# Performance work log

Hardware: AMD Instinct MI355X
Metric: run time of the kernel (lower is better)

## Reference

```python
import jax, jax.numpy as jnp
import numpy as np

D_MODEL = 512
NUM_HEADS = 8
D_K = D_MODEL // NUM_HEADS  # 64, also d_v
SEQ_LEN = 4096


def setup_inputs() -> dict:
    key = jax.random.key(0)
    k1, k2, k3, k4, k5 = jax.random.split(key, 5)
    scale = jnp.float32(1.0 / np.sqrt(D_MODEL))  # keep exp(scores) finite
    return {
        "embeded_seq": jax.random.normal(k1, (SEQ_LEN, D_MODEL), jnp.float32),
        "q_proj": jax.random.normal(k2, (NUM_HEADS, D_MODEL, D_K), jnp.float32) * scale,
        "k_proj": jax.random.normal(k3, (NUM_HEADS, D_MODEL, D_K), jnp.float32) * scale,
        "v_proj": jax.random.normal(k4, (NUM_HEADS, D_MODEL, D_K), jnp.float32) * scale,
        "out_proj": jax.random.normal(k5, (NUM_HEADS * D_K, D_MODEL), jnp.float32) * scale,
    }


def reference(embeded_seq, q_proj, k_proj, v_proj, out_proj):
    # Per-head linear projections: (S, D) x (H, D, d_k) -> (H, S, d_k)
    qs = jnp.einsum("sd,hdk->hsk", embeded_seq, q_proj)
    ks = jnp.einsum("sd,hdk->hsk", embeded_seq, k_proj)
    vs = jnp.einsum("sd,hdv->hsv", embeded_seq, v_proj)

    # Scores: (H, S, S), scaled by sqrt(d_k)
    scores = jnp.einsum("hsk,htk->hst", qs, ks) / jnp.float32(np.sqrt(D_K))

    # Faithful to the original: torch.sum(e_powered) is a GLOBAL scalar sum
    # over all heads and positions (a buggy "softmax"), not a row softmax.
    e = jnp.exp(scores)
    softmaxed = e / jnp.sum(e)

    # Attention output per head: (H, S, d_v)
    head_attns = jnp.einsum("hst,htv->hsv", softmaxed, vs)

    # Concat heads along feature dim -> (S, H*d_v), then output projection
    concat = jnp.transpose(head_attns, (1, 0, 2)).reshape(SEQ_LEN, NUM_HEADS * D_K)
    return concat @ out_proj
```

## Files before the change

### kernel.cpp

```cpp
#include <hip/hip_runtime.h>
#include <stdint.h>

#define S_LEN 4096
#define DMODEL 512
#define NHEAD 8
#define DK 64
#define SPLIT 4
#define TBLK 64
#define NT ((S_LEN / SPLIT) / TBLK)

#if __has_builtin(__builtin_amdgcn_exp2f)
#define EXPFN(x) __builtin_amdgcn_exp2f(x)
#define QSCALE 0.18033688011112042f
#else
#define EXPFN(x) __expf(x)
#define QSCALE 0.125f
#endif

typedef __attribute__((ext_vector_type(8))) short short8;
typedef __attribute__((ext_vector_type(4))) float f32x4;
typedef __attribute__((ext_vector_type(16))) float f32x16;
typedef __attribute__((ext_vector_type(4))) unsigned int uint4v;

__device__ __forceinline__ unsigned short f2bf(float f) {
    unsigned int u = __float_as_uint(f);
    u = (u + 0x7fffu + ((u >> 16) & 1u)) >> 16;
    return (unsigned short)u;
}

__device__ __forceinline__ void gload16(const unsigned short* g, unsigned short* l) {
    __builtin_amdgcn_global_load_lds(
        (const __attribute__((address_space(1))) unsigned int*)g,
        (__attribute__((address_space(3))) unsigned int*)l, 16, 0, 0);
}

__global__ __launch_bounds__(256) void prep_kernel(
    const float* __restrict__ emb,
    const float* __restrict__ wq, const float* __restrict__ wk, const float* __restrict__ wv,
    const float* __restrict__ wo,
    unsigned short* __restrict__ embB,
    unsigned short* __restrict__ oq, unsigned short* __restrict__ ok,
    unsigned short* __restrict__ ov, unsigned short* __restrict__ woT,
    float* __restrict__ Z) {
    __shared__ float tile[64][65];
    const int blk = blockIdx.x, tid = threadIdx.x;
    if (blk < 2048) {
        int i = blk * 256 + tid;
        if (i == 0) *Z = 0.0f;
        float4 v = reinterpret_cast<const float4*>(emb)[i];
        ushort4 o;
        o.x = f2bf(v.x); o.y = f2bf(v.y); o.z = f2bf(v.z); o.w = f2bf(v.w);
        reinterpret_cast<ushort4*>(embB)[i] = o;
        return;
    }
    const int tr = tid >> 4, tc4 = (tid & 15) * 4;
    if (blk < 2240) {
        int idx = blk - 2048;
        int xx = idx & 7, yy = idx >> 3;
        int p = yy >> 3, h = yy & 7;
        const float* in = ((p == 0) ? wq : (p == 1) ? wk : wv) + (size_t)h * DMODEL * DK;
        unsigned short* out = ((p == 0) ? oq : (p == 1) ? ok : ov) + (size_t)h * DK * DMODEL;
        int r0 = xx * 64;
#pragma unroll
        for (int rr = 0; rr < 4; ++rr) {
            float4 v = *reinterpret_cast<const float4*>(in + (size_t)(r0 + tr + rr * 16) * DK + tc4);
            tile[tr + rr * 16][tc4 + 0] = v.x;
            tile[tr + rr * 16][tc4 + 1] = v.y;
            tile[tr + rr * 16][tc4 + 2] = v.z;
            tile[tr + rr * 16][tc4 + 3] = v.w;
        }
        __syncthreads();
#pragma unroll
        for (int rr = 0; rr < 4; ++rr) {
            const int c = tr + rr * 16;
            ushort4 o;
            o.x = f2bf(tile[tc4 + 0][c]);
            o.y = f2bf(tile[tc4 + 1][c]);
            o.z = f2bf(tile[tc4 + 2][c]);
            o.w = f2bf(tile[tc4 + 3][c]);
            *reinterpret_cast<ushort4*>(out + (size_t)c * DMODEL + r0 + tc4) = o;
        }
        return;
    }
    {
        int idx = blk - 2240;
        int c0 = (idx & 7) * 64, r0 = (idx >> 3) * 64;
#pragma unroll
        for (int rr = 0; rr < 4; ++rr) {
            float4 v = *reinterpret_cast<const float4*>(wo + (size_t)(r0 + tr + rr * 16) * DMODEL + c0 + tc4);
            tile[tr + rr * 16][tc4 + 0] = v.x;
            tile[tr + rr * 16][tc4 + 1] = v.y;
            tile[tr + rr * 16][tc4 + 2] = v.z;
            tile[tr + rr * 16][tc4 + 3] = v.w;
        }
        __syncthreads();
#pragma unroll
        for (int rr = 0; rr < 4; ++rr) {
            const int c = tr + rr * 16;
            ushort4 o;
            o.x = f2bf(tile[tc4 + 0][c]);
            o.y = f2bf(tile[tc4 + 1][c]);
            o.z = f2bf(tile[tc4 + 2][c]);
            o.w = f2bf(tile[tc4 + 3][c]);
            *reinterpret_cast<ushort4*>(woT + (size_t)(c0 + c) * DMODEL + r0 + tc4) = o;
        }
    }
}

__global__ __launch_bounds__(256, 2) void proj_tiled_kernel(
    const unsigned short* __restrict__ A,
    const unsigned short* __restrict__ BTall,
    unsigned short* __restrict__ Qo,
    unsigned short* __restrict__ Ko,
    unsigned short* __restrict__ Vo) {
    __shared__ unsigned short lds[32768];
    const int tid = threadIdx.x;
    const int w = tid >> 6, l = tid & 63;
    const int l15 = l & 15, lg = l >> 4;
    const int wr = w >> 1, wc = w & 1;
    const int m0 = blockIdx.x * 128, n0 = blockIdx.y * 128;
    const int srow = l >> 3;
    const int schk = ((l & 7) ^ srow) << 3;
    f32x4 acc[4][4] = {};
    {
        unsigned short* ab = &lds[0];
        unsigned short* bb = &lds[8192];
#pragma unroll
        for (int g = 0; g < 4; ++g) {
            gload16(A + (size_t)(m0 + w * 32 + g * 8 + srow) * DMODEL + schk,
                    ab + (w * 32 + g * 8) * 64);
            gload16(BTall + (size_t)(n0 + w * 32 + g * 8 + srow) * DMODEL + schk,
                    bb + (w * 32 + g * 8) * 64);
        }
    }
    __syncthreads();
    for (int kt = 0; kt < 8; ++kt) {
        const int b = (kt & 1) * 16384;
        if (kt + 1 < 8) {
            const int nb = ((kt + 1) & 1) * 16384;
            const int k0 = (kt + 1) * 64;
            unsigned short* ab = &lds[nb];
            unsigned short* bb = &lds[nb + 8192];
#pragma unroll
            for (int g = 0; g < 4; ++g) {
                gload16(A + (size_t)(m0 + w * 32 + g * 8 + srow) * DMODEL + k0 + schk,
                        ab + (w * 32 + g * 8) * 64);
                gload16(BTall + (size_t)(n0 + w * 32 + g * 8 + srow) * DMODEL + k0 + schk,
                        bb + (w * 32 + g * 8) * 64);
            }
        }
#pragma unroll
        for (int kk = 0; kk < 2; ++kk) {
            short8 am[4], bn[4];
#pragma unroll
            for (int mi = 0; mi < 4; ++mi) {
                const int row = wr * 64 + mi * 16 + l15;
                am[mi] = *reinterpret_cast<const short8*>(
                    &lds[b + row * 64 + ((kk * 32 + lg * 8) ^ ((row & 7) << 3))]);
            }
#pragma unroll
            for (int ni = 0; ni < 4; ++ni) {
                const int row = wc * 64 + ni * 16 + l15;
                bn[ni] = *reinterpret_cast<const short8*>(
                    &lds[b + 8192 + row * 64 + ((kk * 32 + lg * 8) ^ ((row & 7) << 3))]);
            }
#pragma unroll
            for (int mi = 0; mi < 4; ++mi)
#pragma unroll
                for (int ni = 0; ni < 4; ++ni)
                    acc[mi][ni] = __builtin_amdgcn_mfma_f32_16x16x32_bf16(am[mi], bn[ni], acc[mi][ni], 0, 0, 0);
        }
        __syncthreads();
    }
#pragma unroll
    for (int ni = 0; ni < 4; ++ni) {
        const int n = n0 + wc * 64 + ni * 16;
        const int p = n >> 9, h = (n >> 6) & 7, vb = n & 63;
        unsigned short* dst = ((p == 0) ? Qo : (p == 1) ? Ko : Vo) + (size_t)h * S_LEN * DK;
        const float sc = (p == 0) ? QSCALE : 1.0f;
#pragma unroll
        for (int mi = 0; mi < 4; ++mi) {
            const int s = m0 + wr * 64 + mi * 16 + lg * 4;
#pragma unroll
            for (int r = 0; r < 4; ++r)
                dst[(size_t)(s + r) * DK + vb + l15] = f2bf(acc[mi][ni][r] * sc);
        }
    }
}

__global__ __launch_bounds__(256) void vt_kernel(const unsigned short* __restrict__ Vb,
                                                 unsigned short* __restrict__ VT) {
    __shared__ unsigned short tile[4096];
    int h = blockIdx.y, t0 = blockIdx.x * 64;
    const unsigned short* Vh = Vb + h * (S_LEN * DK);
    unsigned short* VTh = VT + h * (DK * S_LEN);
    int c8 = (threadIdx.x & 7) * 8, rw = threadIdx.x >> 3;
#pragma unroll
    for (int rr = 0; rr < 2; ++rr) {
        int t = rw + rr * 32;
        short8 v = *reinterpret_cast<const short8*>(Vh + (t0 + t) * DK + c8);
        *reinterpret_cast<short8*>(&tile[t * 64 + (c8 ^ ((t & 7) << 3))]) = v;
    }
    __syncthreads();
    const int g16 = c8 & ~15;
    const int h4 = (c8 & 8) ? 4 : 0;
#pragma unroll
    for (int rr = 0; rr < 2; ++rr) {
        int v = rw + rr * 32;
        short8 s;
#pragma unroll
        for (int i = 0; i < 8; ++i) {
            int t = g16 + h4 + ((i < 4) ? i : (i + 4));
            s[i] = (short)tile[t * 64 + (v ^ ((t & 7) << 3))];
        }
        *reinterpret_cast<short8*>(VTh + v * S_LEN + t0 + c8) = s;
    }
}

__device__ __forceinline__ void make_pfrag(const f32x16& s, short8 pf[2],
                                           float& z0, float& z1) {
    float p[16];
#pragma unroll
    for (int r = 0; r < 16; ++r) p[r] = EXPFN(s[r]);
#pragma unroll
    for (int r = 0; r < 16; r += 2) { z0 += p[r]; z1 += p[r + 1]; }
    unsigned int c[8];
#pragma unroll
    for (int j = 0; j < 8; ++j)
        asm("v_cvt_pk_bf16_f32 %0, %1, %2" : "=v"(c[j]) : "v"(p[2 * j]), "v"(p[2 * j + 1]));
    uint4v wa = {c[0], c[1], c[2], c[3]};
    uint4v wb = {c[4], c[5], c[6], c[7]};
    pf[0] = __builtin_bit_cast(short8, wa);
    pf[1] = __builtin_bit_cast(short8, wb);
}

__global__ __launch_bounds__(256, 2) void attn_kernel(
    const unsigned short* __restrict__ Qg,
    const unsigned short* __restrict__ Kg,
    const unsigned short* __restrict__ VTg,
    unsigned short* __restrict__ Opart,
    float* __restrict__ Z) {
    __shared__ unsigned short lds[16384];
    const int tid = threadIdx.x;
    const int w = tid >> 6, l = tid & 63;
    const int l31 = l & 31, lh = l >> 5;
    const int vx = l31 & 7;
    const int qb = blockIdx.x, h = blockIdx.y, sp = blockIdx.z;
    const unsigned short* Qh = Qg + h * (S_LEN * DK);
    const unsigned short* Kh = Kg + h * (S_LEN * DK);
    const unsigned short* VTh = VTg + h * (DK * S_LEN);
    const int t_base = sp * (S_LEN / SPLIT);
    const int q0 = qb * 256 + w * 64;

    short8 bq[2][4];
#pragma unroll
    for (int qc = 0; qc < 2; ++qc)
#pragma unroll
        for (int ks = 0; ks < 4; ++ks)
            bq[qc][ks] = *reinterpret_cast<const short8*>(
                Qh + (q0 + qc * 32 + l31) * DK + ks * 16 + lh * 8);

    f32x16 oacc[2][2] = {};
    float z0 = 0.0f, z1 = 0.0f;

    const int srow = l >> 3;
    const int scol = ((l & 7) ^ srow) << 3;
    const unsigned short* gk = Kh + (size_t)(t_base + w * 16 + srow) * DK + scol;
    const unsigned short* gv0 = VTh + (size_t)(w * 16 + srow) * S_LEN + t_base + scol;
    const unsigned short* gv1 = gv0 + 8 * S_LEN;

    {
        unsigned short* kb = &lds[w * 1024];
        gload16(gk, kb);
        gload16(gk + 512, kb + 512);
        unsigned short* vb = &lds[4096 + w * 1024];
        gload16(gv0, vb);
        gload16(gv1, vb + 512);
        gk += 64 * DK; gv0 += 64; gv1 += 64;
    }
    __syncthreads();

    for (int it = 0; it < NT; ++it) {
        const int b = (it & 1) * 8192;
        if (it + 1 < NT) {
            const int nb = ((it + 1) & 1) * 8192;
            unsigned short* kb = &lds[nb + w * 1024];
            gload16(gk, kb);
            gload16(gk + 512, kb + 512);
            unsigned short* vb = &lds[nb + 4096 + w * 1024];
            gload16(gv0, vb);
            gload16(gv1, vb + 512);
            gk += 64 * DK; gv0 += 64; gv1 += 64;
        }
#pragma unroll
        for (int tc = 0; tc < 2; ++tc) {
            f32x16 s0 = {}, s1 = {};
            const int tA = tc * 32 + l31;
            __builtin_amdgcn_s_setprio(1);
#pragma unroll
            for (int ks = 0; ks < 4; ++ks) {
                short8 ka = *reinterpret_cast<const short8*>(
                    &lds[b + tA * 64 + ((ks * 16 + lh * 8) ^ ((tA & 7) << 3))]);
                s0 = __builtin_amdgcn_mfma_f32_32x32x16_bf16(ka, bq[0][ks], s0, 0, 0, 0);
                s1 = __builtin_amdgcn_mfma_f32_32x32x16_bf16(ka, bq[1][ks], s1, 0, 0, 0);
            }
            __builtin_amdgcn_s_setprio(0);
            short8 bv[2][2];
#pragma unroll
            for (int sub = 0; sub < 2; ++sub) {
                const int chk = (tc * 2 + sub) * 2 + lh;
#pragma unroll
                for (int vc = 0; vc < 2; ++vc) {
                    const int v = vc * 32 + l31;
                    bv[sub][vc] = *reinterpret_cast<const short8*>(
                        &lds[b + 4096 + v * 64 + ((chk ^ vx) << 3)]);
                }
            }
            short8 pf0[2], pf1[2];
            make_pfrag(s0, pf0, z0, z1);
#pragma unroll
            for (int sub = 0; sub < 2; ++sub)
#pragma unroll
                for (int vc = 0; vc < 2; ++vc)
                    oacc[0][vc] = __builtin_amdgcn_mfma_f32_32x32x16_bf16(pf0[sub], bv[sub][vc], oacc[0][vc], 0, 0, 0);
            make_pfrag(s1, pf1, z0, z1);
            __builtin_amdgcn_s_setprio(1);
#pragma unroll
            for (int sub = 0; sub < 2; ++sub)
#pragma unroll
                for (int vc = 0; vc < 2; ++vc)
                    oacc[1][vc] = __builtin_amdgcn_mfma_f32_32x32x16_bf16(pf1[sub], bv[sub][vc], oacc[1][vc], 0, 0, 0);
            __builtin_amdgcn_s_setprio(0);
        }
        __syncthreads();
    }
    unsigned short* Op = Opart + ((size_t)(sp * NHEAD + h) * S_LEN + q0) * DK;
#pragma unroll
    for (int qc = 0; qc < 2; ++qc)
#pragma unroll
        for (int vc = 0; vc < 2; ++vc)
#pragma unroll
            for (int reg = 0; reg < 16; ++reg) {
                int q = qc * 32 + (reg & 3) + 8 * (reg >> 2) + 4 * lh;
                Op[(size_t)q * DK + vc * 32 + l31] = f2bf(oacc[qc][vc][reg]);
            }
    float zloc = z0 + z1;
#pragma unroll
    for (int off = 32; off > 0; off >>= 1) zloc += __shfl_xor(zloc, off, 64);
    if (l == 0) atomicAdd(Z, zloc);
}

__global__ __launch_bounds__(256) void reduce_o_kernel(
    const unsigned short* __restrict__ Opart, unsigned short* __restrict__ cc) {
    const int HSV = NHEAD * S_LEN * DK;
    int i = blockIdx.x * blockDim.x + threadIdx.x;
    if (i * 4 >= HSV) return;
    float s0 = 0, s1 = 0, s2 = 0, s3 = 0;
#pragma unroll
    for (int sp = 0; sp < SPLIT; ++sp) {
        ushort4 v = *reinterpret_cast<const ushort4*>(&Opart[(size_t)sp * HSV + i * 4]);
        s0 += __uint_as_float((unsigned int)v.x << 16);
        s1 += __uint_as_float((unsigned int)v.y << 16);
        s2 += __uint_as_float((unsigned int)v.z << 16);
        s3 += __uint_as_float((unsigned int)v.w << 16);
    }
    int e = i * 4;
    int h = e / (S_LEN * DK);
    int rem = e - h * (S_LEN * DK);
    int srow = rem / DK;
    int v = rem - srow * DK;
    ushort4 o4;
    o4.x = f2bf(s0); o4.y = f2bf(s1); o4.z = f2bf(s2); o4.w = f2bf(s3);
    *reinterpret_cast<ushort4*>(&cc[srow * DMODEL + h * DK + v]) = o4;
}

__global__ __launch_bounds__(256, 2) void out_tiled_kernel(
    const unsigned short* __restrict__ A,
    const unsigned short* __restrict__ BT,
    const float* __restrict__ Z,
    float* __restrict__ Cout) {
    __shared__ unsigned short lds[32768];
    const int tid = threadIdx.x;
    const int w = tid >> 6, l = tid & 63;
    const int l15 = l & 15, lg = l >> 4;
    const int wr = w >> 1, wc = w & 1;
    const int m0 = blockIdx.x * 128, n0 = blockIdx.y * 128;
    const int srow = l >> 3;
    const int schk = ((l & 7) ^ srow) << 3;
    const float invZ = 1.0f / *Z;
    f32x4 acc[4][4] = {};
    {
        unsigned short* ab = &lds[0];
        unsigned short* bb = &lds[8192];
#pragma unroll
        for (int g = 0; g < 4; ++g) {
            gload16(A + (size_t)(m0 + w * 32 + g * 8 + srow) * DMODEL + schk,
                    ab + (w * 32 + g * 8) * 64);
            gload16(BT + (size_t)(n0 + w * 32 + g * 8 + srow) * DMODEL + schk,
                    bb + (w * 32 + g * 8) * 64);
        }
    }
    __syncthreads();
    for (int kt = 0; kt < 8; ++kt) {
        const int b = (kt & 1) * 16384;
        if (kt + 1 < 8) {
            const int nb = ((kt + 1) & 1) * 16384;
            const int k0 = (kt + 1) * 64;
            unsigned short* ab = &lds[nb];
            unsigned short* bb = &lds[nb + 8192];
#pragma unroll
            for (int g = 0; g < 4; ++g) {
                gload16(A + (size_t)(m0 + w * 32 + g * 8 + srow) * DMODEL + k0 + schk,
                        ab + (w * 32 + g * 8) * 64);
                gload16(BT + (size_t)(n0 + w * 32 + g * 8 + srow) * DMODEL + k0 + schk,
                        bb + (w * 32 + g * 8) * 64);
            }
        }
#pragma unroll
        for (int kk = 0; kk < 2; ++kk) {
            short8 am[4], bn[4];
#pragma unroll
            for (int mi = 0; mi < 4; ++mi) {
                const int row = wr * 64 + mi * 16 + l15;
                am[mi] = *reinterpret_cast<const short8*>(
                    &lds[b + row * 64 + ((kk * 32 + lg * 8) ^ ((row & 7) << 3))]);
            }
#pragma unroll
            for (int ni = 0; ni < 4; ++ni) {
                const int row = wc * 64 + ni * 16 + l15;
                bn[ni] = *reinterpret_cast<const short8*>(
                    &lds[b + 8192 + row * 64 + ((kk * 32 + lg * 8) ^ ((row & 7) << 3))]);
            }
#pragma unroll
            for (int mi = 0; mi < 4; ++mi)
#pragma unroll
                for (int ni = 0; ni < 4; ++ni)
                    acc[mi][ni] = __builtin_amdgcn_mfma_f32_16x16x32_bf16(am[mi], bn[ni], acc[mi][ni], 0, 0, 0);
        }
        __syncthreads();
    }
#pragma unroll
    for (int ni = 0; ni < 4; ++ni) {
        const int n = n0 + wc * 64 + ni * 16;
#pragma unroll
        for (int mi = 0; mi < 4; ++mi) {
            const int s = m0 + wr * 64 + mi * 16 + lg * 4;
#pragma unroll
            for (int r = 0; r < 4; ++r)
                Cout[(size_t)(s + r) * DMODEL + n + l15] = acc[mi][ni][r] * invZ;
        }
    }
}


extern "C" void kernel_launch(void* const* d_in, const int* in_sizes, int n_in,
                              void* d_out, int out_size, void* d_ws, size_t ws_size,
                              hipStream_t stream) {
    const float* emb = (const float*)d_in[0];
    const float* wq = (const float*)d_in[1];
    const float* wk = (const float*)d_in[2];
    const float* wv = (const float*)d_in[3];
    const float* wo = (const float*)d_in[4];
    float* out = (float*)d_out;
    char* ws = (char*)d_ws;
    unsigned short* embB = (unsigned short*)(ws);
    unsigned short* wqT  = (unsigned short*)(ws + 4194304);
    unsigned short* wkT  = (unsigned short*)(ws + 4718592);
    unsigned short* wvT  = (unsigned short*)(ws + 5242880);
    unsigned short* woT  = (unsigned short*)(ws + 5767168);
    unsigned short* Qb   = (unsigned short*)(ws + 6291456);
    unsigned short* Kb   = (unsigned short*)(ws + 10485760);
    unsigned short* Vb   = (unsigned short*)(ws + 14680064);
    unsigned short* cc   = (unsigned short*)(ws + 18874368);
    float* Z             = (float*)(ws + 23068672);
    unsigned short* Opart = (unsigned short*)(ws + 23072768);
    unsigned short* VT   = embB;

    prep_kernel<<<2304, 256, 0, stream>>>(emb, wq, wk, wv, wo, embB, wqT, wkT, wvT, woT, Z);
    proj_tiled_kernel<<<dim3(32, 12), 256, 0, stream>>>(embB, wqT, Qb, Kb, Vb);
    vt_kernel<<<dim3(64, 8), 256, 0, stream>>>(Vb, VT);
    attn_kernel<<<dim3(16, 8, SPLIT), 256, 0, stream>>>(Qb, Kb, VT, Opart, Z);
    reduce_o_kernel<<<2048, 256, 0, stream>>>(Opart, cc);
    out_tiled_kernel<<<dim3(32, 4), 256, 0, stream>>>(cc, woT, Z, out);
}
```

Baseline: 92.04 us.

## Software-pipeline second-half PV MFMAs into next iteration of attention loop

Unrolls the two 32-key sub-tiles of each 64-key tile and defers the P·V MFMAs of the second sub-tile into the start of the next iteration, keeping the P fragments and V operands in registers across the barrier. An epilogue after the loop flushes the last deferred MFMAs. This is meant to overlap exp/pack work with independent matrix ops and reduce stalls around the barrier and softmax. It raises register pressure, which can lower occupancy or cause spills.

```diff
diff --git a/kernel.cpp b/kernel.cpp
--- a/kernel.cpp
+++ b/kernel.cpp
@@ -262,6 +262,8 @@
 
     f32x16 oacc[2][2] = {};
     float z0 = 0.0f, z1 = 0.0f;
+    short8 pfP[2][2];
+    short8 bvP[2][2];
 
     const int srow = l >> 3;
     const int scol = ((l & 7) ^ srow) << 3;
@@ -292,10 +294,20 @@
             gload16(gv1, vb + 512);
             gk += 64 * DK; gv0 += 64; gv1 += 64;
         }
-#pragma unroll
-        for (int tc = 0; tc < 2; ++tc) {
+        if (it > 0) {
+            __builtin_amdgcn_s_setprio(1);
+#pragma unroll
+            for (int sub = 0; sub < 2; ++sub)
+#pragma unroll
+                for (int vc = 0; vc < 2; ++vc) {
+                    oacc[0][vc] = __builtin_amdgcn_mfma_f32_32x32x16_bf16(pfP[0][sub], bvP[sub][vc], oacc[0][vc], 0, 0, 0);
+                    oacc[1][vc] = __builtin_amdgcn_mfma_f32_32x32x16_bf16(pfP[1][sub], bvP[sub][vc], oacc[1][vc], 0, 0, 0);
+                }
+            __builtin_amdgcn_s_setprio(0);
+        }
+        {
             f32x16 s0 = {}, s1 = {};
-            const int tA = tc * 32 + l31;
+            const int tA = l31;
             __builtin_amdgcn_s_setprio(1);
 #pragma unroll
             for (int ks = 0; ks < 4; ++ks) {
@@ -308,7 +320,7 @@
             short8 bv[2][2];
 #pragma unroll
             for (int sub = 0; sub < 2; ++sub) {
-                const int chk = (tc * 2 + sub) * 2 + lh;
+                const int chk = sub * 2 + lh;
 #pragma unroll
                 for (int vc = 0; vc < 2; ++vc) {
                     const int v = vc * 32 + l31;
@@ -332,7 +344,41 @@
                     oacc[1][vc] = __builtin_amdgcn_mfma_f32_32x32x16_bf16(pf1[sub], bv[sub][vc], oacc[1][vc], 0, 0, 0);
             __builtin_amdgcn_s_setprio(0);
         }
+        {
+            f32x16 s0 = {}, s1 = {};
+            const int tA = 32 + l31;
+            __builtin_amdgcn_s_setprio(1);
+#pragma unroll
+            for (int ks = 0; ks < 4; ++ks) {
+                short8 ka = *reinterpret_cast<const short8*>(
+                    &lds[b + tA * 64 + ((ks * 16 + lh * 8) ^ ((tA & 7) << 3))]);
+                s0 = __builtin_amdgcn_mfma_f32_32x32x16_bf16(ka, bq[0][ks], s0, 0, 0, 0);
+                s1 = __builtin_amdgcn_mfma_f32_32x32x16_bf16(ka, bq[1][ks], s1, 0, 0, 0);
+            }
+            __builtin_amdgcn_s_setprio(0);
+#pragma unroll
+            for (int sub = 0; sub < 2; ++sub) {
+                const int chk = (2 + sub) * 2 + lh;
+#pragma unroll
+                for (int vc = 0; vc < 2; ++vc) {
+                    const int v = vc * 32 + l31;
+                    bvP[sub][vc] = *reinterpret_cast<const short8*>(
+                        &lds[b + 4096 + v * 64 + ((chk ^ vx) << 3)]);
+                }
+            }
+            make_pfrag(s0, pfP[0], z0, z1);
+            make_pfrag(s1, pfP[1], z0, z1);
+        }
         __syncthreads();
+    }
+    {
+#pragma unroll
+        for (int sub = 0; sub < 2; ++sub)
+#pragma unroll
+            for (int vc = 0; vc < 2; ++vc) {
+                oacc[0][vc] = __builtin_amdgcn_mfma_f32_32x32x16_bf16(pfP[0][sub], bvP[sub][vc], oacc[0][vc], 0, 0, 0);
+                oacc[1][vc] = __builtin_amdgcn_mfma_f32_32x32x16_bf16(pfP[1][sub], bvP[sub][vc], oacc[1][vc], 0, 0, 0);
+            }
     }
     unsigned short* Op = Opart + ((size_t)(sp * NHEAD + h) * S_LEN + q0) * DK;
 #pragma unroll
```

After: 92.87 us. About the same (+0.9%).
